# Optimization experiments

Hardware: AMD Instinct MI355X
Metric: run time of the kernel (lower is better)

The kernel has to match this reference:

```python
import jax, jax.numpy as jnp
import numpy as np
from jax import lax

STATE_DIM = 256
INPUT_DIM = 1
OUTPUT_DIM = 1
KX = 5
BSZ = 896
SEQ_LEN = 1024


def setup_inputs() -> dict:
    key = jax.random.key(0)
    kx_, ka, kb, kc, km = jax.random.split(key, 5)
    x = jax.random.normal(kx_, (BSZ, SEQ_LEN, INPUT_DIM), dtype=jnp.float32)
    # exponential_decay_init(lam=5): decay factors in (e^-5, 1)
    A = jnp.exp(-5.0 * jax.random.uniform(ka, (STATE_DIM,), dtype=jnp.float32))
    Bp = jax.random.normal(kb, (INPUT_DIM, STATE_DIM), dtype=jnp.float32) / INPUT_DIM
    C = jax.random.normal(kc, (STATE_DIM, OUTPUT_DIM), dtype=jnp.float32) / STATE_DIM
    M = jax.random.normal(km, (OUTPUT_DIM, INPUT_DIM, KX), dtype=jnp.float32) / INPUT_DIM
    h0 = jnp.zeros((STATE_DIM,), dtype=jnp.float32)
    return {"x": x, "A": A, "Bp": Bp, "C": C, "M": M, "h0": h0}


def reference(x, A, Bp, C, M, h0):
    # x: [B, T, I]; A: [S]; Bp: [I, S]; C: [S, O]; M: [O, I, K]; h0: [S]
    Bsz, T, I = x.shape
    S = A.shape[0]

    # Diagonal linear recurrence: h_t = h_{t-1} * A + x_t @ Bp, y_t = h_t @ C
    xb = jnp.einsum('bti,is->tbs', x, Bp)  # precompute input projections [T,B,S]

    def step(h, xb_t):
        h = h * A + xb_t
        return h, h @ C  # y_t: [B, O]

    h_init = jnp.broadcast_to(h0, (Bsz, S))
    _, ys = lax.scan(step, h_init, xb)          # ys: [T, B, O]
    lds_out = jnp.swapaxes(ys, 0, 1)            # [B, T, O]

    # AR tap: ar[b,t,o] = sum_{k<K, i} x[b, t-k, i] * M[o, i, k] (causal, zero-padded)
    K = M.shape[2]
    Mf = M[:, :, ::-1]                           # flip kernel for correlation conv
    ar = lax.conv_general_dilated(
        jnp.swapaxes(x, 1, 2),                   # [B, I, T]
        Mf,                                      # [O, I, K]
        window_strides=(1,),
        padding=[(K - 1, 0)],
        dimension_numbers=('NCH', 'OIH', 'NCH'),
    )                                            # [B, O, T]
    ar = jnp.swapaxes(ar, 1, 2)                  # [B, T, O]

    return lds_out + ar
```

## Files before the change

### kernel.cpp

```cpp
#include <hip/hip_runtime.h>


#define T_LEN 1024
#define BSZ_N 896
#define S_DIM 256
#define KX_N  5
#define TBLK  512
#define NTB   (T_LEN / TBLK)
#define XS_CHUNKS 392
#define RED_WAVES 3
#define THR2  1.6e-5f

__device__ __forceinline__ int swz(int u) { return u ^ ((u >> 3) & 7); }

#define CSEL(v, c) ((c)==0?(v).x:((c)==1?(v).y:((c)==2?(v).z:(v).w)))

#define FMA_STEP(F0,F1,P0,P1,KA,KB) do {                                         \
    const float kv[8] = {(KA).x,(KA).y,(KA).z,(KA).w,(KB).x,(KB).y,(KB).z,(KB).w};\
    _Pragma("unroll")                                                             \
    for (int tt = 0; tt < 8; ++tt) {                                              \
        _Pragma("unroll")                                                         \
        for (int j = 0; j < 8; ++j) {                                             \
            const int e = tt - j;                                                 \
            const float xv = (e >= 4) ? CSEL(P1, e-4)                             \
                           : (e >= 0) ? CSEL(P0, e)                               \
                           : (e >= -4) ? CSEL(F1, e+4)                            \
                           : CSEL(F0, e+8);                                       \
            acc[tt] = fmaf(kv[j], xv, acc[tt]);                                   \
        }                                                                         \
    }                                                                             \
} while (0)

#define LOAD_PAIR(D0, D1, U) do {                                                 \
    const int ba_ = swz(U) << 4;                                                  \
    D0 = *(const float4*)((const char*)xs + ba_);                                 \
    D1 = *(const float4*)((const char*)xs + (ba_ ^ 16));                          \
} while (0)

__global__ __launch_bounds__(256)
void k_build(const float* __restrict__ A, const float* __restrict__ Bp,
             const float* __restrict__ C, const float* __restrict__ M,
             float* __restrict__ Kg) {
    const int d = blockIdx.x;
    const int s = threadIdx.x;
    const float w = C[s] * Bp[s];
    const float ad = exp2f((float)d * log2f(A[s]));
    float v = w * ad;
#pragma unroll
    for (int off = 1; off < 64; off <<= 1) v += __shfl_xor(v, off, 64);
    __shared__ float part[4];
    const int wave = threadIdx.x >> 6;
    const int lane = threadIdx.x & 63;
    if (lane == 0) part[wave] = v;
    __syncthreads();
    if (threadIdx.x == 0) {
        float r = part[0] + part[1] + part[2] + part[3];
        if (d < KX_N) r += M[d];
        Kg[d] = r;
    }
}

__global__ __launch_bounds__(256)
void k_conv(const float* __restrict__ x, const float* __restrict__ Kg,
            float* __restrict__ out) {
    __shared__ __align__(16) float xs[XS_CHUNKS * 4];
    __shared__ __align__(16) float red[RED_WAVES][64][9];
    __shared__ float seg8[8];
    const int tb  = (NTB - 1) - blockIdx.x;
    const int b   = blockIdx.y;
    const int t0  = tb * TBLK;
    const int tid = threadIdx.x;
    const int wave = tid >> 6, lane = tid & 63;

    {
        const float4 kv = *(const float4*)(Kg + 4 * tid);
        float es = kv.x * kv.x + kv.y * kv.y + kv.z * kv.z + kv.w * kv.w;
#pragma unroll
        for (int off = 1; off < 32; off <<= 1) es += __shfl_xor(es, off, 32);
        if ((tid & 31) == 0) seg8[tid >> 5] = es;
    }
    __syncthreads();

    float suf = 0.f;
    int m = 8;
#pragma unroll
    for (int i = 7; i >= 1; --i) {
        suf += seg8[i];
        if (suf <= THR2) m = i;
    }
    const int Dq  = 16 * m;
    const int Cq  = (t0 + TBLK) / 8;
    const int Cqe = (Cq < Dq) ? Cq : Dq;

    const float* xb = x + b * T_LEN;
    const int tau0 = t0 - 1032;
    const int j_lo0 = 256 - 2 * Cqe - 2;
    const int j_lo  = (j_lo0 > 0) ? j_lo0 : 0;
    for (int j = j_lo + tid; j < XS_CHUNKS; j += 256) {
        const int tau = tau0 + 4 * j;
        float4 v = make_float4(0.f, 0.f, 0.f, 0.f);
        if ((unsigned)tau < (unsigned)T_LEN) v = *(const float4*)(xb + tau);
        *(float4*)(xs + 4 * swz(j)) = v;
    }
    __syncthreads();

    float acc[8];
#pragma unroll
    for (int k = 0; k < 8; ++k) acc[k] = 0.f;

    const int n   = Cqe / 4;
    const int n4  = n / 4;
    const int qu0 = __builtin_amdgcn_readfirstlane(wave * n);
    const float* __restrict__ Kw = Kg + 8 * qu0;
    const int ub0 = 256 + 2 * lane - 2 * qu0;

    float4 p0, p1;
    LOAD_PAIR(p0, p1, ub0 + 2);

    for (int i = 0; i < n4; ++i) {
        const int ui = ub0 - 8 * i;
        const float* __restrict__ Ki = Kw + 32 * i;
        float4 a0, a1, b0, b1, c0, c1, d0, d1;
        LOAD_PAIR(a0, a1, ui);
        LOAD_PAIR(b0, b1, ui - 2);
        LOAD_PAIR(c0, c1, ui - 4);
        LOAD_PAIR(d0, d1, ui - 6);
        {
            const float4 ka = *(const float4*)(Ki);
            const float4 kb = *(const float4*)(Ki + 4);
            FMA_STEP(a0, a1, p0, p1, ka, kb);
        }
        {
            const float4 ka = *(const float4*)(Ki + 8);
            const float4 kb = *(const float4*)(Ki + 12);
            FMA_STEP(b0, b1, a0, a1, ka, kb);
        }
        {
            const float4 ka = *(const float4*)(Ki + 16);
            const float4 kb = *(const float4*)(Ki + 20);
            FMA_STEP(c0, c1, b0, b1, ka, kb);
        }
        {
            const float4 ka = *(const float4*)(Ki + 24);
            const float4 kb = *(const float4*)(Ki + 28);
            FMA_STEP(d0, d1, c0, c1, ka, kb);
        }
        p0 = d0; p1 = d1;
    }

    if (wave != 0) {
#pragma unroll
        for (int k = 0; k < 8; ++k) red[wave - 1][lane][k] = acc[k];
    }
    __syncthreads();
    if (wave == 0) {
#pragma unroll
        for (int w = 0; w < RED_WAVES; ++w)
#pragma unroll
            for (int k = 0; k < 8; ++k) acc[k] += red[w][lane][k];
        float* op = out + b * T_LEN + t0 + 8 * lane;
        float4 o0 = {acc[0], acc[1], acc[2], acc[3]};
        float4 o1 = {acc[4], acc[5], acc[6], acc[7]};
        *(float4*)op       = o0;
        *(float4*)(op + 4) = o1;
    }
}

extern "C" void kernel_launch(void* const* d_in, const int* in_sizes, int n_in,
                              void* d_out, int out_size, void* d_ws, size_t ws_size,
                              hipStream_t stream) {
    const float* x  = (const float*)d_in[0];
    const float* A  = (const float*)d_in[1];
    const float* Bp = (const float*)d_in[2];
    const float* C  = (const float*)d_in[3];
    const float* M  = (const float*)d_in[4];
    float* out = (float*)d_out;
    float* Kg  = (float*)d_ws;

    k_build<<<dim3(T_LEN), dim3(S_DIM), 0, stream>>>(A, Bp, C, M, Kg);
    k_conv <<<dim3(NTB, BSZ_N), dim3(256), 0, stream>>>(x, Kg, out);
}
```

Before: 18.28 us.

## Process full sequence per block, splitting waves across time halves and kernel depth

Each block now handles a whole batch row (1024 outputs) instead of half a row. Waves are split two by two across the time halves and across halves of the truncated kernel depth, with a pairwise reduction through shared memory. The row's input is staged once into a larger shared buffer, and those loads are issued before the energy-threshold reduction so their latency overlaps it. The aim is to stop loading the overlapping input window twice and to halve the block count, at the cost of fewer blocks (896) for occupancy and more LDS per block.

```diff
diff --git a/kernel.cpp b/kernel.cpp
--- a/kernel.cpp
+++ b/kernel.cpp
@@ -5,10 +5,7 @@
 #define BSZ_N 896
 #define S_DIM 256
 #define KX_N  5
-#define TBLK  512
-#define NTB   (T_LEN / TBLK)
-#define XS_CHUNKS 392
-#define RED_WAVES 3
+#define XS_CHUNKS 516
 #define THR2  1.6e-5f
 
 __device__ __forceinline__ int swz(int u) { return u ^ ((u >> 3) & 7); }
@@ -64,21 +61,33 @@
 void k_conv(const float* __restrict__ x, const float* __restrict__ Kg,
             float* __restrict__ out) {
     __shared__ __align__(16) float xs[XS_CHUNKS * 4];
-    __shared__ __align__(16) float red[RED_WAVES][64][9];
+    __shared__ __align__(16) float red[2][64][9];
     __shared__ float seg8[8];
-    const int tb  = (NTB - 1) - blockIdx.x;
-    const int b   = blockIdx.y;
-    const int t0  = tb * TBLK;
+    const int b   = blockIdx.x;
     const int tid = threadIdx.x;
     const int wave = tid >> 6, lane = tid & 63;
+    const int th = wave >> 1;
+    const int dh = wave & 1;
+
+    const float4 kv = *(const float4*)(Kg + 4 * tid);
+    const int j1 = 130 + tid;
+    const int j2 = j1 + 256;
+    const int tau1 = 4 * j1 - 1032;
+    const int tau2 = 4 * j2 - 1032;
+    float4 v1 = make_float4(0.f, 0.f, 0.f, 0.f);
+    float4 v2 = make_float4(0.f, 0.f, 0.f, 0.f);
+    const float* xb = x + b * T_LEN;
+    if (tau1 >= 0) v1 = *(const float4*)(xb + tau1);
+    if (j2 < 514)  v2 = *(const float4*)(xb + tau2);
 
     {
-        const float4 kv = *(const float4*)(Kg + 4 * tid);
         float es = kv.x * kv.x + kv.y * kv.y + kv.z * kv.z + kv.w * kv.w;
 #pragma unroll
         for (int off = 1; off < 32; off <<= 1) es += __shfl_xor(es, off, 32);
         if ((tid & 31) == 0) seg8[tid >> 5] = es;
     }
+    *(float4*)(xs + 4 * swz(j1)) = v1;
+    if (j2 < 514) *(float4*)(xs + 4 * swz(j2)) = v2;
     __syncthreads();
 
     float suf = 0.f;
@@ -89,30 +98,18 @@
         if (suf <= THR2) m = i;
     }
     const int Dq  = 16 * m;
-    const int Cq  = (t0 + TBLK) / 8;
+    const int Cq  = (th == 0) ? 64 : 128;
     const int Cqe = (Cq < Dq) ? Cq : Dq;
-
-    const float* xb = x + b * T_LEN;
-    const int tau0 = t0 - 1032;
-    const int j_lo0 = 256 - 2 * Cqe - 2;
-    const int j_lo  = (j_lo0 > 0) ? j_lo0 : 0;
-    for (int j = j_lo + tid; j < XS_CHUNKS; j += 256) {
-        const int tau = tau0 + 4 * j;
-        float4 v = make_float4(0.f, 0.f, 0.f, 0.f);
-        if ((unsigned)tau < (unsigned)T_LEN) v = *(const float4*)(xb + tau);
-        *(float4*)(xs + 4 * swz(j)) = v;
-    }
-    __syncthreads();
+    const int n   = Cqe >> 1;
+    const int n4  = n >> 2;
 
     float acc[8];
 #pragma unroll
     for (int k = 0; k < 8; ++k) acc[k] = 0.f;
 
-    const int n   = Cqe / 4;
-    const int n4  = n / 4;
-    const int qu0 = __builtin_amdgcn_readfirstlane(wave * n);
+    const int qu0 = __builtin_amdgcn_readfirstlane(dh * n);
     const float* __restrict__ Kw = Kg + 8 * qu0;
-    const int ub0 = 256 + 2 * lane - 2 * qu0;
+    const int ub0 = 128 * th + 2 * lane + 256 - 2 * qu0;
 
     float4 p0, p1;
     LOAD_PAIR(p0, p1, ub0 + 2);
@@ -148,17 +145,15 @@
         p0 = d0; p1 = d1;
     }
 
-    if (wave != 0) {
+    if (dh) {
 #pragma unroll
-        for (int k = 0; k < 8; ++k) red[wave - 1][lane][k] = acc[k];
+        for (int k = 0; k < 8; ++k) red[th][lane][k] = acc[k];
     }
     __syncthreads();
-    if (wave == 0) {
+    if (!dh) {
 #pragma unroll
-        for (int w = 0; w < RED_WAVES; ++w)
-#pragma unroll
-            for (int k = 0; k < 8; ++k) acc[k] += red[w][lane][k];
-        float* op = out + b * T_LEN + t0 + 8 * lane;
+        for (int k = 0; k < 8; ++k) acc[k] += red[th][lane][k];
+        float* op = out + b * T_LEN + 512 * th + 8 * lane;
         float4 o0 = {acc[0], acc[1], acc[2], acc[3]};
         float4 o1 = {acc[4], acc[5], acc[6], acc[7]};
         *(float4*)op       = o0;
@@ -178,5 +173,5 @@
     float* Kg  = (float*)d_ws;
 
     k_build<<<dim3(T_LEN), dim3(S_DIM), 0, stream>>>(A, Bp, C, M, Kg);
-    k_conv <<<dim3(NTB, BSZ_N), dim3(256), 0, stream>>>(x, Kg, out);
+    k_conv <<<dim3(BSZ_N), dim3(256), 0, stream>>>(x, Kg, out);
 }
```

Result: slower. 19.45 us (+6.4%).
